# Kernel tuning notes

Hardware: AMD Instinct MI355X
Metric: run time of the kernel (lower is better)

Reference implementation:

```python
import jax, jax.numpy as jnp
import numpy as np

N = 65536        # nodes
E = 131072       # directed edges
D = 512          # emb_dim
L = 5            # num_layer
G = 512          # num graphs
EPS = 1e-5       # batchnorm eps
NUM_ATOM_TYPE, NUM_CHIRALITY = 120, 3
NUM_BOND_TYPE, NUM_BOND_DIR = 6, 3


def setup_inputs() -> dict:
    key = jax.random.key(0)
    ks = jax.random.split(key, 12)
    s = 0.02
    return {
        "x": jax.random.randint(ks[0], (N, 2), 0, 3),
        "edge_index": jax.random.randint(ks[1], (2, E), 0, N),
        "edge_attr": jax.random.randint(ks[2], (E, 2), 0, 3),
        "batch": jnp.sort(jax.random.randint(ks[3], (N,), 0, G)),
        "x_emb1": jax.random.normal(ks[4], (NUM_ATOM_TYPE, D), jnp.float32) * s,
        "x_emb2": jax.random.normal(ks[5], (NUM_CHIRALITY, D), jnp.float32) * s,
        "e_emb1": jax.random.normal(ks[6], (L, NUM_BOND_TYPE, D), jnp.float32) * s,
        "e_emb2": jax.random.normal(ks[7], (L, NUM_BOND_DIR, D), jnp.float32) * s,
        "W1": jax.random.normal(ks[8], (L, D, 2 * D), jnp.float32) * s,
        "b1": jnp.zeros((L, 2 * D), jnp.float32),
        "W2": jax.random.normal(ks[9], (L, 2 * D, D), jnp.float32) * s,
        "b2": jnp.zeros((L, D), jnp.float32),
        "gamma": jnp.ones((L, D), jnp.float32),
        "beta": jnp.zeros((L, D), jnp.float32),
    }


def reference(x, edge_index, edge_attr, batch,
              x_emb1, x_emb2, e_emb1, e_emb2,
              W1, b1, W2, b2, gamma, beta):
    n = x.shape[0]
    # atom embedding: type + chirality
    h = x_emb1[x[:, 0]] + x_emb2[x[:, 1]]                     # [N, D]

    # add self loops (appended after real edges, attr = [4, 0])
    loops = jnp.arange(n)
    src = jnp.concatenate([edge_index[0], loops])             # [E+N]
    dst = jnp.concatenate([edge_index[1], loops])
    sl_attr = jnp.concatenate(
        [jnp.full((n, 1), 4, dtype=edge_attr.dtype),
         jnp.zeros((n, 1), dtype=edge_attr.dtype)], axis=1)
    ea = jnp.concatenate([edge_attr, sl_attr], axis=0)        # [E+N, 2]

    for l in range(L):
        # per-edge embedding: bond type + bond direction
        e = e_emb1[l][ea[:, 0]] + e_emb2[l][ea[:, 1]]         # [E+N, D]
        msg = h[src] + e                                      # gather + add
        agg = jax.ops.segment_sum(msg, dst, num_segments=n)   # scatter-add
        # GIN MLP: Linear(D,2D) -> ReLU -> Linear(2D,D)
        hh = jax.nn.relu(agg @ W1[l] + b1[l]) @ W2[l] + b2[l]
        # BatchNorm1d (training-mode batch statistics)
        mean = hh.mean(axis=0)
        var = hh.var(axis=0)
        hh = (hh - mean) * jax.lax.rsqrt(var + EPS) * gamma[l] + beta[l]
        if l < L - 1:
            hh = jax.nn.relu(hh)   # dropout(p=0) is identity
        h = hh

    # JK='last': node rep = h; graph rep = global mean pool over batch ids
    counts = jax.ops.segment_sum(jnp.ones((n,), h.dtype), batch, num_segments=G)
    graph = jax.ops.segment_sum(h, batch, num_segments=G) / jnp.maximum(counts, 1.0)[:, None]
    return graph, h
```

## Files before the change

### kernel.cpp

```cpp
#include <hip/hip_runtime.h>
#include <stdint.h>

#define Nn 65536
#define Ee 131072
#define Dd 512
#define D2 1024
#define Ll 5
#define Gg 512
#define EPSf 1e-5f

typedef _Float16 f16x8 __attribute__((ext_vector_type(8)));
typedef float f32x4 __attribute__((ext_vector_type(4)));
typedef unsigned short u16x8 __attribute__((ext_vector_type(8)));

__device__ __forceinline__ unsigned short f2h(float f) {
    _Float16 h = (_Float16)f;
    union { _Float16 h; unsigned short u; } c; c.h = h;
    return c.u;
}

__device__ __forceinline__ float h2f(unsigned short s) {
    union { unsigned short s; _Float16 h; } c; c.s = s;
    return (float)c.h;
}

__device__ __forceinline__ void gload_lds16(const void* g, void* l) {
    __builtin_amdgcn_global_load_lds(
        (const __attribute__((address_space(1))) void*)(uintptr_t)g,
        (__attribute__((address_space(3))) void*)(unsigned)(uintptr_t)l,
        16, 0, 0);
}

__global__ void k_transW(const float* __restrict__ src, unsigned short* __restrict__ dst,
                         int K, int Nw) {
    long total = (long)Ll * K * Nw;
    for (long idx = (long)blockIdx.x * blockDim.x + threadIdx.x; idx < total;
         idx += (long)gridDim.x * blockDim.x) {
        long l = idx / ((long)K * Nw);
        long rem = idx - l * (long)K * Nw;
        int k = (int)(rem / Nw), n = (int)(rem % Nw);
        dst[(l * Nw + n) * K + k] = f2h(src[idx]);
    }
}

__global__ void k_etab(const float* __restrict__ ee1, const float* __restrict__ ee2,
                       float* __restrict__ E) {
    int idx = blockIdx.x * blockDim.x + threadIdx.x;
    const int total = Ll * 18 * Dd;
    if (idx < total) {
        int l = idx / (18 * Dd);
        int rem = idx - l * 18 * Dd;
        int j = rem / Dd, c = rem - j * Dd;
        int a0 = j / 3, a1 = j - a0 * 3;
        E[idx] = ee1[((size_t)l * 6 + a0) * Dd + c] + ee2[((size_t)l * 3 + a1) * Dd + c];
    }
}

__global__ void k_embed(const int* __restrict__ x,
                        const float* __restrict__ xe1, const float* __restrict__ xe2,
                        unsigned short* __restrict__ hhf) {
    const int total = Nn * 64;
    for (int idx = blockIdx.x * blockDim.x + threadIdx.x; idx < total;
         idx += gridDim.x * blockDim.x) {
        int node = idx >> 6, c8 = (idx & 63) * 8;
        int t0 = x[2 * node], t1 = x[2 * node + 1];
        const float4* p1 = (const float4*)(xe1 + (size_t)t0 * Dd + c8);
        const float4* p2 = (const float4*)(xe2 + (size_t)t1 * Dd + c8);
        float4 a0 = p1[0], a1 = p1[1], b0 = p2[0], b1 = p2[1];
        u16x8 o;
        o[0] = f2h(a0.x + b0.x); o[1] = f2h(a0.y + b0.y);
        o[2] = f2h(a0.z + b0.z); o[3] = f2h(a0.w + b0.w);
        o[4] = f2h(a1.x + b1.x); o[5] = f2h(a1.y + b1.y);
        o[6] = f2h(a1.z + b1.z); o[7] = f2h(a1.w + b1.w);
        *(u16x8*)(hhf + (size_t)node * Dd + c8) = o;
    }
}

__global__ void k_zeroN(int* __restrict__ p, int n) {
    int i = blockIdx.x * blockDim.x + threadIdx.x;
    if (i < n) p[i] = 0;
}

__global__ void k_hist(const int* __restrict__ edst, int* __restrict__ cnt) {
    int e = blockIdx.x * blockDim.x + threadIdx.x;
    if (e < Ee) atomicAdd(&cnt[edst[e]], 1);
}

__global__ void k_scan(const int* __restrict__ cnt, int* __restrict__ off,
                       int* __restrict__ cursor) {
    __shared__ int part[1024];
    int t = threadIdx.x;
    int base = t * 64;
    int s = 0;
    for (int i = 0; i < 64; ++i) s += cnt[base + i];
    part[t] = s;
    __syncthreads();
    for (int d = 1; d < 1024; d <<= 1) {
        int v = (t >= d) ? part[t - d] : 0;
        __syncthreads();
        part[t] += v;
        __syncthreads();
    }
    int run = part[t] - s;
    for (int i = 0; i < 64; ++i) {
        off[base + i] = run;
        cursor[base + i] = run;
        run += cnt[base + i];
    }
    if (t == 1023) off[Nn] = run;
}

__global__ void k_place(const int* __restrict__ esrc, const int* __restrict__ edst,
                        const int* __restrict__ eattr, int* __restrict__ cursor,
                        int* __restrict__ ckey, int* __restrict__ csrc) {
    int e = blockIdx.x * blockDim.x + threadIdx.x;
    if (e < Ee) {
        int d = edst[e];
        int p = atomicAdd(&cursor[d], 1);
        ckey[p] = e * 32 + (eattr[2 * e] * 3 + eattr[2 * e + 1]);
        csrc[p] = esrc[e];
    }
}

__global__ void k_sort(const int* __restrict__ off, int* __restrict__ ckey,
                       int* __restrict__ csrc) {
    int node = blockIdx.x * blockDim.x + threadIdx.x;
    if (node >= Nn) return;
    int kb = off[node], ke = off[node + 1];
    for (int i = kb + 1; i < ke; ++i) {
        int k = ckey[i], s = csrc[i];
        int j = i - 1;
        while (j >= kb && ckey[j] > k) {
            ckey[j + 1] = ckey[j]; csrc[j + 1] = csrc[j]; --j;
        }
        ckey[j + 1] = k; csrc[j + 1] = s;
    }
}

template <int NORM>
__global__ __launch_bounds__(256) void k_gather(const unsigned short* __restrict__ hf16,
                                                const float* __restrict__ ss,
                                                const int* __restrict__ off,
                                                const int* __restrict__ ckey,
                                                const int* __restrict__ csrc,
                                                const float* __restrict__ El,
                                                unsigned short* __restrict__ aggh) {
    int node = (blockIdx.x << 2) + (threadIdx.x >> 6);
    int lane = threadIdx.x & 63;
    int c8 = lane * 8;
    float sa[8], sb[8];
    if (NORM) {
        float4 a0 = *(const float4*)(ss + c8), a1 = *(const float4*)(ss + c8 + 4);
        float4 b0 = *(const float4*)(ss + 512 + c8), b1 = *(const float4*)(ss + 512 + c8 + 4);
        sa[0] = a0.x; sa[1] = a0.y; sa[2] = a0.z; sa[3] = a0.w;
        sa[4] = a1.x; sa[5] = a1.y; sa[6] = a1.z; sa[7] = a1.w;
        sb[0] = b0.x; sb[1] = b0.y; sb[2] = b0.z; sb[3] = b0.w;
        sb[4] = b1.x; sb[5] = b1.y; sb[6] = b1.z; sb[7] = b1.w;
    }
    float acc[8];
    {
        u16x8 v = *(const u16x8*)(hf16 + (size_t)node * Dd + c8);
        float4 e0 = *(const float4*)(El + 12 * Dd + c8);
        float4 e1 = *(const float4*)(El + 12 * Dd + c8 + 4);
        float ev[8];
        ev[0] = e0.x; ev[1] = e0.y; ev[2] = e0.z; ev[3] = e0.w;
        ev[4] = e1.x; ev[5] = e1.y; ev[6] = e1.z; ev[7] = e1.w;
#pragma unroll
        for (int i = 0; i < 8; ++i) {
            float hv = h2f(v[i]);
            if (NORM) hv = fmaxf(fmaf(hv, sa[i], sb[i]), 0.f);
            acc[i] = hv + ev[i];
        }
    }
    int kb = off[node], ke = off[node + 1];
    for (int k = kb; k < ke; ++k) {
        int src = csrc[k];
        int at = ckey[k] & 31;
        u16x8 v = *(const u16x8*)(hf16 + (size_t)src * Dd + c8);
        const float* Er = El + (size_t)at * Dd + c8;
        float4 e0 = *(const float4*)(Er);
        float4 e1 = *(const float4*)(Er + 4);
        float ev[8];
        ev[0] = e0.x; ev[1] = e0.y; ev[2] = e0.z; ev[3] = e0.w;
        ev[4] = e1.x; ev[5] = e1.y; ev[6] = e1.z; ev[7] = e1.w;
#pragma unroll
        for (int i = 0; i < 8; ++i) {
            float hv = h2f(v[i]);
            if (NORM) hv = fmaxf(fmaf(hv, sa[i], sb[i]), 0.f);
            acc[i] += hv + ev[i];
        }
    }
    u16x8 o;
#pragma unroll
    for (int i = 0; i < 8; ++i) o[i] = f2h(acc[i]);
    *(u16x8*)(aggh + (size_t)node * Dd + c8) = o;
}

__device__ __forceinline__ void stage_h(const unsigned short* __restrict__ g, int ldk,
                                        long row0, int col0, char* region, int tid) {
    int wbase = (tid >> 6) << 10;
#pragma unroll
    for (int r = 0; r < 2; ++r) {
        int gi = tid + r * 512;
        int row = gi >> 2;
        int k16 = (gi & 3) ^ ((row >> 1) & 3);
        gload_lds16(g + (row0 + row) * (long)ldk + col0 + k16 * 8,
                    region + r * 8192 + wbase);
    }
}

__device__ __forceinline__ f16x8 rd_frag(const char* region, int row, int l4) {
    int slot = l4 ^ ((row >> 1) & 3);
    return *(const f16x8*)(region + row * 64 + (slot << 4));
}

template <int EPI>
__global__ __launch_bounds__(512, 2) void gemm_dp(const unsigned short* __restrict__ A,
                                                  const unsigned short* __restrict__ BT,
                                                  const float* __restrict__ bias,
                                                  unsigned short* __restrict__ Cb,
                                                  float* __restrict__ pS,
                                                  int M, int N, int K) {
    __shared__ __align__(16) char lds[131072];
    const int tid = threadIdx.x;
    const int lane = tid & 63;
    const int w = tid >> 6;
    const int wm = w >> 2, wn = w & 3;
    const int l15 = lane & 15, l4 = lane >> 4;

    const int nwg = gridDim.x;
    const int cpx = nwg >> 3;
    const int bid = blockIdx.x;
    const int wg = (bid & 7) * cpx + (bid >> 3);
    const int ntn = N >> 8;
    const long bm = (long)(wg / ntn) * 256;
    const long bn = (long)(wg % ntn) * 256;

    const int NT = K >> 5;

    f32x4 acc[8][4];
#pragma unroll
    for (int i = 0; i < 8; ++i)
#pragma unroll
        for (int j = 0; j < 4; ++j) acc[i][j] = (f32x4){0.f, 0.f, 0.f, 0.f};

    stage_h(A, K, bm, 0, lds, tid);
    stage_h(BT, K, bn, 0, lds + 16384, tid);
    stage_h(A, K, bm, 32, lds + 32768, tid);
    stage_h(BT, K, bn, 32, lds + 32768 + 16384, tid);
    stage_h(A, K, bm, 64, lds + 65536, tid);
    stage_h(BT, K, bn, 64, lds + 65536 + 16384, tid);
    asm volatile("s_waitcnt vmcnt(8)" ::: "memory");
    __builtin_amdgcn_s_barrier();
    asm volatile("" ::: "memory");

    for (int t = 0; t < NT; ++t) {
        const char* Ac = lds + (size_t)(t & 3) * 32768;
        const char* Bc = Ac + 16384;
        f16x8 af[8], bv[4];
#pragma unroll
        for (int fn = 0; fn < 4; ++fn)
            bv[fn] = rd_frag(Bc, wn * 64 + fn * 16 + l15, l4);
#pragma unroll
        for (int fm = 0; fm < 8; ++fm)
            af[fm] = rd_frag(Ac, wm * 128 + fm * 16 + l15, l4);
        if (t + 3 < NT) {
            char* dst = lds + (size_t)((t + 3) & 3) * 32768;
            stage_h(A, K, bm, (t + 3) * 32, dst, tid);
            stage_h(BT, K, bn, (t + 3) * 32, dst + 16384, tid);
        }
#pragma unroll
        for (int fm = 0; fm < 8; ++fm)
#pragma unroll
            for (int fn = 0; fn < 4; ++fn)
                acc[fm][fn] = __builtin_amdgcn_mfma_f32_16x16x32_f16(af[fm], bv[fn], acc[fm][fn], 0, 0, 0);
        if (t + 3 < NT) {
            asm volatile("s_waitcnt vmcnt(8)" ::: "memory");
        } else if (t + 2 < NT) {
            asm volatile("s_waitcnt vmcnt(4)" ::: "memory");
        } else if (t + 1 < NT) {
            asm volatile("s_waitcnt vmcnt(0)" ::: "memory");
        }
        __builtin_amdgcn_s_barrier();
        asm volatile("" ::: "memory");
    }

    unsigned short* cl = (unsigned short*)lds;
    float cs[4] = {0.f, 0.f, 0.f, 0.f}, cq[4] = {0.f, 0.f, 0.f, 0.f};
#pragma unroll
    for (int hh = 0; hh < 2; ++hh) {
        __syncthreads();
        if (wm == hh) {
#pragma unroll
            for (int fn = 0; fn < 4; ++fn) {
                int col = wn * 64 + fn * 16 + l15;
                float bval = bias[bn + col];
#pragma unroll
                for (int fm = 0; fm < 8; ++fm) {
                    int r0 = fm * 16 + l4 * 4;
#pragma unroll
                    for (int r = 0; r < 4; ++r) {
                        float v = acc[fm][fn][r] + bval;
                        if (EPI == 0) v = fmaxf(v, 0.f);
                        else { cs[fn] += v; cq[fn] += v * v; }
                        cl[(r0 + r) * 264 + col] = f2h(v);
                    }
                }
            }
        }
        __syncthreads();
#pragma unroll
        for (int i = 0; i < 8; ++i) {
            int g = tid + i * 512;
            int r = g >> 5, cg = (g & 31) << 3;
            u16x8 val = *(const u16x8*)&cl[r * 264 + cg];
            *(u16x8*)&Cb[(bm + hh * 128 + r) * N + bn + cg] = val;
        }
    }
    if (EPI == 1) {
#pragma unroll
        for (int fn = 0; fn < 4; ++fn) {
            float s = cs[fn], q = cq[fn];
            s += __shfl_xor(s, 16); s += __shfl_xor(s, 32);
            q += __shfl_xor(q, 16); q += __shfl_xor(q, 32);
            if (l4 == 0) {
                int col = (int)bn + wn * 64 + fn * 16 + l15;
                int rowgrp = ((int)(bm >> 8)) * 2 + wm;
                pS[rowgrp * 512 + col] = s;
                pS[262144 + rowgrp * 512 + col] = q;
            }
        }
    }
}

__global__ void k_bnA(const float* __restrict__ pS, float* __restrict__ pT) {
    int b = blockIdx.x;
    int t = threadIdx.x;
    float s0 = 0.f, s1 = 0.f, q0 = 0.f, q1 = 0.f;
#pragma unroll
    for (int i = 0; i < 8; ++i) {
        int rg = b * 8 + i;
        s0 += pS[rg * 512 + t];
        s1 += pS[rg * 512 + t + 256];
        q0 += pS[262144 + rg * 512 + t];
        q1 += pS[262144 + rg * 512 + t + 256];
    }
    pT[b * 512 + t] = s0;
    pT[b * 512 + t + 256] = s1;
    pT[32768 + b * 512 + t] = q0;
    pT[32768 + b * 512 + t + 256] = q1;
}

__global__ void k_bnB(const float* __restrict__ pT, const float* __restrict__ gamma,
                      const float* __restrict__ beta, float* __restrict__ ss) {
    int c = threadIdx.x;
    float s = 0.f, q = 0.f;
    for (int b = 0; b < 64; ++b) {
        s += pT[b * 512 + c];
        q += pT[32768 + b * 512 + c];
    }
    float mean = s * (1.f / (float)Nn);
    float var = q * (1.f / (float)Nn) - mean * mean;
    float a = gamma[c] * rsqrtf(var + EPSf);
    ss[c] = a;
    ss[512 + c] = beta[c] - mean * a;
}

__global__ void k_norm(const unsigned short* __restrict__ hhf, const float* __restrict__ ss,
                       float4* __restrict__ h4) {
    const int total = Nn * 128;
    const float4* ss4 = (const float4*)ss;
    for (int idx = blockIdx.x * blockDim.x + threadIdx.x; idx < total;
         idx += gridDim.x * blockDim.x) {
        int c = idx & 127;
        ushort4 u = *(const ushort4*)(hhf + (size_t)idx * 4);
        float4 v = make_float4(h2f(u.x), h2f(u.y), h2f(u.z), h2f(u.w));
        float4 a = ss4[c], b = ss4[128 + c];
        v.x = fmaf(v.x, a.x, b.x); v.y = fmaf(v.y, a.y, b.y);
        v.z = fmaf(v.z, a.z, b.z); v.w = fmaf(v.w, a.w, b.w);
        h4[idx] = v;
    }
}

__global__ void k_pool(const unsigned short* __restrict__ hhf, const float* __restrict__ ss,
                       const int* __restrict__ batch, float* __restrict__ graph) {
    int g = blockIdx.x, t = threadIdx.x;
    int lo = 0, hi = Nn;
    while (lo < hi) { int m = (lo + hi) >> 1; if (batch[m] < g) lo = m + 1; else hi = m; }
    int s = lo;
    lo = s; hi = Nn;
    while (lo < hi) { int m = (lo + hi) >> 1; if (batch[m] <= g) lo = m + 1; else hi = m; }
    int e = lo;
    float a0 = ss[t], a1 = ss[t + 256];
    float b0 = ss[512 + t], b1 = ss[512 + t + 256];
    float s0 = 0.f, s1 = 0.f;
    for (int r = s; r < e; ++r) {
        const unsigned short* row = hhf + (size_t)r * Dd;
        s0 += fmaf(h2f(row[t]), a0, b0);
        s1 += fmaf(h2f(row[t + 256]), a1, b1);
    }
    int cnt = e - s; if (cnt < 1) cnt = 1;
    float inv = 1.f / (float)cnt;
    graph[(long)g * Dd + t] = s0 * inv;
    graph[(long)g * Dd + t + 256] = s1 * inv;
}

extern "C" void kernel_launch(void* const* d_in, const int* in_sizes, int n_in,
                              void* d_out, int out_size, void* d_ws, size_t ws_size,
                              hipStream_t stream) {
    (void)in_sizes; (void)n_in; (void)out_size; (void)ws_size;
    const int* x      = (const int*)d_in[0];
    const int* ei     = (const int*)d_in[1];
    const int* ea     = (const int*)d_in[2];
    const int* batch  = (const int*)d_in[3];
    const float* xe1  = (const float*)d_in[4];
    const float* xe2  = (const float*)d_in[5];
    const float* ee1  = (const float*)d_in[6];
    const float* ee2  = (const float*)d_in[7];
    const float* W1   = (const float*)d_in[8];
    const float* b1   = (const float*)d_in[9];
    const float* W2   = (const float*)d_in[10];
    const float* b2   = (const float*)d_in[11];
    const float* gamma = (const float*)d_in[12];
    const float* beta  = (const float*)d_in[13];

    float* graph = (float*)d_out;
    float* h = graph + (size_t)Gg * Dd;

    char* w = (char*)d_ws;
    int* csr_off = (int*)w;                     w += (Nn + 1) * 4;
    int* cursor = (int*)w;                      w += Nn * 4;
    int* cnt = (int*)w;                         w += Nn * 4;
    int* ckey = (int*)w;                        w += Ee * 4;
    int* csrc = (int*)w;                        w += Ee * 4;
    float* ss = (float*)w;                      w += 4096;
    float* pS = (float*)w;                      w += 2 * 512 * 512 * 4;
    float* pT = (float*)w;                      w += 2 * 64 * 512 * 4;
    float* Etab = (float*)w;                    w += (size_t)Ll * 18 * Dd * 4;
    unsigned short* aggh = (unsigned short*)w;  w += (size_t)Nn * Dd * 2;
    unsigned short* hhf = (unsigned short*)w;   w += (size_t)Nn * Dd * 2;
    unsigned short* w1t = (unsigned short*)w;   w += (size_t)Ll * D2 * Dd * 2;
    unsigned short* w2t = (unsigned short*)w;   w += (size_t)Ll * Dd * D2 * 2;

    k_transW<<<2048, 256, 0, stream>>>(W1, w1t, Dd, D2);
    k_transW<<<2048, 256, 0, stream>>>(W2, w2t, D2, Dd);
    k_etab<<<(Ll * 18 * Dd + 255) / 256, 256, 0, stream>>>(ee1, ee2, Etab);
    k_embed<<<2048, 256, 0, stream>>>(x, xe1, xe2, hhf);

    k_zeroN<<<64, 1024, 0, stream>>>(cnt, Nn);
    k_hist<<<Ee / 256, 256, 0, stream>>>(ei + Ee, cnt);
    k_scan<<<1, 1024, 0, stream>>>(cnt, csr_off, cursor);
    k_place<<<Ee / 256, 256, 0, stream>>>(ei, ei + Ee, ea, cursor, ckey, csrc);
    k_sort<<<Nn / 256, 256, 0, stream>>>(csr_off, ckey, csrc);

    for (int l = 0; l < Ll; ++l) {
        const float* El = Etab + (size_t)l * 18 * Dd;
        if (l == 0)
            k_gather<0><<<Nn / 4, 256, 0, stream>>>(hhf, nullptr, csr_off, ckey, csrc,
                                                    El, aggh);
        else
            k_gather<1><<<Nn / 4, 256, 0, stream>>>(hhf, ss, csr_off, ckey, csrc,
                                                    El, aggh);
        gemm_dp<0><<<(Nn / 256) * (D2 / 256), 512, 0, stream>>>(
            aggh, w1t + (size_t)l * D2 * Dd, b1 + (size_t)l * D2,
            (unsigned short*)h, nullptr, Nn, D2, Dd);
        gemm_dp<1><<<(Nn / 256) * (Dd / 256), 512, 0, stream>>>(
            (const unsigned short*)h, w2t + (size_t)l * Dd * D2, b2 + (size_t)l * Dd,
            hhf, pS, Nn, Dd, D2);
        k_bnA<<<64, 256, 0, stream>>>(pS, pT);
        k_bnB<<<1, 512, 0, stream>>>(pT, gamma + (size_t)l * Dd, beta + (size_t)l * Dd, ss);
    }

    k_norm<<<2048, 256, 0, stream>>>(hhf, ss, (float4*)h);
    k_pool<<<Gg, 256, 0, stream>>>(hhf, ss, batch, graph);
}
```

Baseline: 1.437 ms.

## Shrink GEMM tile to 256x128 with 4 waves and triple-buffered LDS

Replaces the 8-wave 256x256 GEMM tile with a 4-wave 256x128 tile, reducing LDS per block from 128KB to 72KB and going from 4-stage to 3-stage prefetch. The smaller LDS footprint lets two blocks co-reside per CU, so one block's epilogue and loads can overlap another's MFMA work. In exchange, B-operand reuse per block drops and the grid doubles, and the BN partial row-group indexing is changed to match the new tile.

```diff
diff --git a/kernel.cpp b/kernel.cpp
--- a/kernel.cpp
+++ b/kernel.cpp
@@ -196,16 +196,29 @@
     *(u16x8*)(aggh + (size_t)node * Dd + c8) = o;
 }
 
-__device__ __forceinline__ void stage_h(const unsigned short* __restrict__ g, int ldk,
+__device__ __forceinline__ void stage_a(const unsigned short* __restrict__ g, int ldk,
                                         long row0, int col0, char* region, int tid) {
     int wbase = (tid >> 6) << 10;
 #pragma unroll
-    for (int r = 0; r < 2; ++r) {
-        int gi = tid + r * 512;
+    for (int r = 0; r < 4; ++r) {
+        int gi = tid + r * 256;
         int row = gi >> 2;
         int k16 = (gi & 3) ^ ((row >> 1) & 3);
         gload_lds16(g + (row0 + row) * (long)ldk + col0 + k16 * 8,
-                    region + r * 8192 + wbase);
+                    region + r * 4096 + wbase);
+    }
+}
+
+__device__ __forceinline__ void stage_b(const unsigned short* __restrict__ g, int ldk,
+                                        long row0, int col0, char* region, int tid) {
+    int wbase = (tid >> 6) << 10;
+#pragma unroll
+    for (int r = 0; r < 2; ++r) {
+        int gi = tid + r * 256;
+        int row = gi >> 2;
+        int k16 = (gi & 3) ^ ((row >> 1) & 3);
+        gload_lds16(g + (row0 + row) * (long)ldk + col0 + k16 * 8,
+                    region + r * 4096 + wbase);
     }
 }
 
@@ -215,26 +228,26 @@
 }
 
 template <int EPI>
-__global__ __launch_bounds__(512, 2) void gemm_dp(const unsigned short* __restrict__ A,
+__global__ __launch_bounds__(256, 2) void gemm_ov(const unsigned short* __restrict__ A,
                                                   const unsigned short* __restrict__ BT,
                                                   const float* __restrict__ bias,
                                                   unsigned short* __restrict__ Cb,
                                                   float* __restrict__ pS,
                                                   int M, int N, int K) {
-    __shared__ __align__(16) char lds[131072];
+    __shared__ __align__(16) char lds[73728];
     const int tid = threadIdx.x;
     const int lane = tid & 63;
     const int w = tid >> 6;
-    const int wm = w >> 2, wn = w & 3;
+    const int wm = w >> 1, wn = w & 1;
     const int l15 = lane & 15, l4 = lane >> 4;
 
     const int nwg = gridDim.x;
     const int cpx = nwg >> 3;
     const int bid = blockIdx.x;
     const int wg = (bid & 7) * cpx + (bid >> 3);
-    const int ntn = N >> 8;
+    const int ntn = N >> 7;
     const long bm = (long)(wg / ntn) * 256;
-    const long bn = (long)(wg % ntn) * 256;
+    const long bn = (long)(wg % ntn) * 128;
 
     const int NT = K >> 5;
 
@@ -244,18 +257,17 @@
 #pragma unroll
         for (int j = 0; j < 4; ++j) acc[i][j] = (f32x4){0.f, 0.f, 0.f, 0.f};
 
-    stage_h(A, K, bm, 0, lds, tid);
-    stage_h(BT, K, bn, 0, lds + 16384, tid);
-    stage_h(A, K, bm, 32, lds + 32768, tid);
-    stage_h(BT, K, bn, 32, lds + 32768 + 16384, tid);
-    stage_h(A, K, bm, 64, lds + 65536, tid);
-    stage_h(BT, K, bn, 64, lds + 65536 + 16384, tid);
-    asm volatile("s_waitcnt vmcnt(8)" ::: "memory");
+    stage_a(A, K, bm, 0, lds, tid);
+    stage_b(BT, K, bn, 0, lds + 16384, tid);
+    stage_a(A, K, bm, 32, lds + 24576, tid);
+    stage_b(BT, K, bn, 32, lds + 24576 + 16384, tid);
+    asm volatile("s_waitcnt vmcnt(6)" ::: "memory");
     __builtin_amdgcn_s_barrier();
     asm volatile("" ::: "memory");
 
+    int cur = 0, nx2 = 2;
     for (int t = 0; t < NT; ++t) {
-        const char* Ac = lds + (size_t)(t & 3) * 32768;
+        const char* Ac = lds + cur * 24576;
         const char* Bc = Ac + 16384;
         f16x8 af[8], bv[4];
 #pragma unroll
@@ -264,58 +276,53 @@
 #pragma unroll
         for (int fm = 0; fm < 8; ++fm)
             af[fm] = rd_frag(Ac, wm * 128 + fm * 16 + l15, l4);
-        if (t + 3 < NT) {
-            char* dst = lds + (size_t)((t + 3) & 3) * 32768;
-            stage_h(A, K, bm, (t + 3) * 32, dst, tid);
-            stage_h(BT, K, bn, (t + 3) * 32, dst + 16384, tid);
+        if (t + 2 < NT) {
+            char* dst = lds + nx2 * 24576;
+            stage_a(A, K, bm, (t + 2) * 32, dst, tid);
+            stage_b(BT, K, bn, (t + 2) * 32, dst + 16384, tid);
         }
 #pragma unroll
         for (int fm = 0; fm < 8; ++fm)
 #pragma unroll
             for (int fn = 0; fn < 4; ++fn)
                 acc[fm][fn] = __builtin_amdgcn_mfma_f32_16x16x32_f16(af[fm], bv[fn], acc[fm][fn], 0, 0, 0);
-        if (t + 3 < NT) {
-            asm volatile("s_waitcnt vmcnt(8)" ::: "memory");
-        } else if (t + 2 < NT) {
-            asm volatile("s_waitcnt vmcnt(4)" ::: "memory");
+        if (t + 2 < NT) {
+            asm volatile("s_waitcnt vmcnt(6)" ::: "memory");
         } else if (t + 1 < NT) {
             asm volatile("s_waitcnt vmcnt(0)" ::: "memory");
         }
         __builtin_amdgcn_s_barrier();
         asm volatile("" ::: "memory");
+        cur = (cur == 2) ? 0 : cur + 1;
+        nx2 = (nx2 == 2) ? 0 : nx2 + 1;
     }
 
     unsigned short* cl = (unsigned short*)lds;
     float cs[4] = {0.f, 0.f, 0.f, 0.f}, cq[4] = {0.f, 0.f, 0.f, 0.f};
-#pragma unroll
-    for (int hh = 0; hh < 2; ++hh) {
-        __syncthreads();
-        if (wm == hh) {
-#pragma unroll
-            for (int fn = 0; fn < 4; ++fn) {
-                int col = wn * 64 + fn * 16 + l15;
-                float bval = bias[bn + col];
-#pragma unroll
-                for (int fm = 0; fm < 8; ++fm) {
-                    int r0 = fm * 16 + l4 * 4;
-#pragma unroll
-                    for (int r = 0; r < 4; ++r) {
-                        float v = acc[fm][fn][r] + bval;
-                        if (EPI == 0) v = fmaxf(v, 0.f);
-                        else { cs[fn] += v; cq[fn] += v * v; }
-                        cl[(r0 + r) * 264 + col] = f2h(v);
-                    }
-                }
+    __syncthreads();
+#pragma unroll
+    for (int fn = 0; fn < 4; ++fn) {
+        int col = wn * 64 + fn * 16 + l15;
+        float bval = bias[bn + col];
+#pragma unroll
+        for (int fm = 0; fm < 8; ++fm) {
+            int r0 = wm * 128 + fm * 16 + l4 * 4;
+#pragma unroll
+            for (int r = 0; r < 4; ++r) {
+                float v = acc[fm][fn][r] + bval;
+                if (EPI == 0) v = fmaxf(v, 0.f);
+                else { cs[fn] += v; cq[fn] += v * v; }
+                cl[(r0 + r) * 136 + col] = f2h(v);
             }
         }
-        __syncthreads();
-#pragma unroll
-        for (int i = 0; i < 8; ++i) {
-            int g = tid + i * 512;
-            int r = g >> 5, cg = (g & 31) << 3;
-            u16x8 val = *(const u16x8*)&cl[r * 264 + cg];
-            *(u16x8*)&Cb[(bm + hh * 128 + r) * N + bn + cg] = val;
-        }
+    }
+    __syncthreads();
+#pragma unroll
+    for (int i = 0; i < 16; ++i) {
+        int g = tid + i * 256;
+        int r = g >> 4, cg = (g & 15) << 3;
+        u16x8 val = *(const u16x8*)&cl[r * 136 + cg];
+        *(u16x8*)&Cb[(bm + r) * N + bn + cg] = val;
     }
     if (EPI == 1) {
 #pragma unroll
@@ -325,7 +332,7 @@
             q += __shfl_xor(q, 16); q += __shfl_xor(q, 32);
             if (l4 == 0) {
                 int col = (int)bn + wn * 64 + fn * 16 + l15;
-                int rowgrp = ((int)(bm >> 8)) * 2 + wm;
+                int rowgrp = (int)(bm >> 7) + wm;
                 pS[rowgrp * 512 + col] = s;
                 pS[262144 + rowgrp * 512 + col] = q;
             }
@@ -461,10 +468,10 @@
         else
             k_gather<1><<<Nn / 4, 256, 0, stream>>>(hhf, ss, csr_off, ckey, csrc,
                                                     El, aggh);
-        gemm_dp<0><<<(Nn / 256) * (D2 / 256), 512, 0, stream>>>(
+        gemm_ov<0><<<(Nn / 256) * (D2 / 128), 256, 0, stream>>>(
             aggh, w1t + (size_t)l * D2 * Dd, b1 + (size_t)l * D2,
             (unsigned short*)h, nullptr, Nn, D2, Dd);
-        gemm_dp<1><<<(Nn / 256) * (Dd / 256), 512, 0, stream>>>(
+        gemm_ov<1><<<(Nn / 256) * (Dd / 128), 256, 0, stream>>>(
             (const unsigned short*)h, w2t + (size_t)l * Dd * D2, b2 + (size_t)l * Dd,
             hhf, pS, Nn, Dd, D2);
         k_bnA<<<64, 256, 0, stream>>>(pS, pT);
```

Result: no change. 1.413 ms (-1.6%).
